# Optimization experiments

Hardware: AMD Instinct MI355X
Metric: run time of the kernel (lower is better)

## Reference

```python
import jax, jax.numpy as jnp
import numpy as np

N_HEADS, N_LEVELS, N_POINTS = 8, 4, 4


def _bilinear(im, grid, H, W):
    # im: [N, D, H*W] flattened level feature, grid: [N, Q, P, 2] in [-1, 1]
    # F.grid_sample bilinear, padding_mode='zeros', align_corners=False
    N, Q, P, _ = grid.shape
    D = im.shape[1]
    gx = ((grid[..., 0] + 1.0) * W - 1.0) * 0.5
    gy = ((grid[..., 1] + 1.0) * H - 1.0) * 0.5
    x0f = jnp.floor(gx)
    y0f = jnp.floor(gy)
    x0 = x0f.astype(jnp.int32)
    y0 = y0f.astype(jnp.int32)
    wx1 = gx - x0f
    wy1 = gy - y0f
    acc = jnp.zeros((N, D, Q * P), im.dtype)
    corners = ((0, 0, (1 - wx1) * (1 - wy1)), (1, 0, wx1 * (1 - wy1)),
               (0, 1, (1 - wx1) * wy1), (1, 1, wx1 * wy1))
    for dx, dy, wgt in corners:
        xi = x0 + dx
        yi = y0 + dy
        valid = (xi >= 0) & (xi < W) & (yi >= 0) & (yi < H)
        idx = jnp.clip(yi, 0, H - 1) * W + jnp.clip(xi, 0, W - 1)
        v = jnp.take_along_axis(im, idx.reshape(N, 1, Q * P), axis=2)  # [N,D,QP]
        acc = acc + v * jnp.where(valid, wgt, 0.0).reshape(N, 1, Q * P)
    return acc.reshape(N, D, Q, P)


def _forward(query, value, reference_points, shapes_np,
             w_off, b_off, w_attn, b_attn, w_val, b_val, w_out, b_out):
    B, Q, E = query.shape
    H_, L, P = N_HEADS, N_LEVELS, N_POINTS
    D = E // H_
    v = (value @ w_val + b_val).reshape(B, -1, H_, D)  # [B, Nv, H, D]
    off = (query @ w_off + b_off).reshape(B, Q, H_, L, P, 2)
    attn = (query @ w_attn + b_attn).reshape(B, Q, H_, L * P)
    attn = jax.nn.softmax(attn, axis=-1).reshape(B, Q, H_, L, P)
    # offset_scale = [W_l, H_l] per level
    scale = jnp.asarray(np.stack([shapes_np[:, 1], shapes_np[:, 0]], -1), jnp.float32)
    locs = reference_points[:, :, None, :, None, :] + off / scale[None, None, None, :, None, :]
    grid = 2.0 * locs - 1.0  # [B, Q, H, L, P, 2]
    starts = np.concatenate([[0], np.cumsum(shapes_np[:, 0] * shapes_np[:, 1])]).astype(int)
    out = jnp.zeros((B * H_, D, Q), query.dtype)
    for lvl in range(L):
        h, w = int(shapes_np[lvl, 0]), int(shapes_np[lvl, 1])
        feat = v[:, starts[lvl]:starts[lvl + 1]]                      # [B, h*w, H, D]
        feat = feat.transpose(0, 2, 3, 1).reshape(B * H_, D, h * w)   # [BH, D, hw]
        g = jnp.transpose(grid[:, :, :, lvl], (0, 2, 1, 3, 4)).reshape(B * H_, Q, P, 2)
        sampled = _bilinear(feat, g, h, w)                            # [BH, D, Q, P]
        wl = jnp.transpose(attn[:, :, :, lvl], (0, 2, 1, 3)).reshape(B * H_, 1, Q, P)
        out = out + (sampled * wl).sum(-1)                            # [BH, D, Q]
    out = out.reshape(B, H_ * D, Q).transpose(0, 2, 1)                # [B, Q, E]
    return out @ w_out + b_out


def setup_inputs() -> dict:
    key = jax.random.key(0)
    ks = jax.random.split(key, 12)
    B, Q, E = 2, 19947, 256
    L, H_, P = N_LEVELS, N_HEADS, N_POINTS
    shapes = jnp.array([[100, 150], [50, 75], [25, 38], [13, 19]], dtype=jnp.int64)
    s = 0.02
    return {
        'query': jax.random.normal(ks[0], (B, Q, E), jnp.float32),
        'value': jax.random.normal(ks[1], (B, Q, E), jnp.float32),
        'reference_points': jax.random.uniform(ks[2], (B, Q, L, 2), jnp.float32),
        'spatial_shapes': shapes,
        'w_off': jax.random.normal(ks[3], (E, H_ * L * P * 2), jnp.float32) * s,
        'b_off': jax.random.normal(ks[4], (H_ * L * P * 2,), jnp.float32) * s,
        'w_attn': jax.random.normal(ks[5], (E, H_ * L * P), jnp.float32) * s,
        'b_attn': jax.random.normal(ks[6], (H_ * L * P,), jnp.float32) * s,
        'w_val': jax.random.normal(ks[7], (E, E), jnp.float32) * s,
        'b_val': jax.random.normal(ks[8], (E,), jnp.float32) * s,
        'w_out': jax.random.normal(ks[9], (E, E), jnp.float32) * s,
        'b_out': jax.random.normal(ks[10], (E,), jnp.float32) * s,
    }


def reference(query, value, reference_points, spatial_shapes,
              w_off, b_off, w_attn, b_attn, w_val, b_val, w_out, b_out):
    shapes_np = np.asarray(spatial_shapes)
    return _forward(query, value, reference_points, shapes_np,
                    w_off, b_off, w_attn, b_attn, w_val, b_val, w_out, b_out)
```

## Files before the change

kernel.cpp:

```cpp
#include <hip/hip_runtime.h>
#include <math.h>

#define B_    2
#define Q_    19947
#define E_    256
#define H_    8
#define D_    32
#define L_    4
#define P_    4

typedef _Float16 f16_t;
typedef f16_t f16x8 __attribute__((ext_vector_type(8)));
typedef f16_t f16x4 __attribute__((ext_vector_type(4)));
typedef float f32x4 __attribute__((ext_vector_type(4)));

__global__ __launch_bounds__(256)
void transpose_all(const float* __restrict__ w_val, const float* __restrict__ w_off,
                   const float* __restrict__ w_attn, const float* __restrict__ w_out,
                   f16_t* __restrict__ WtV, f16_t* __restrict__ WtQ,
                   f16_t* __restrict__ WtO)
{
    const float* in; f16_t* out; int N;
    switch (blockIdx.z) {
        case 0:  in = w_val;  out = WtV;             N = 256; break;
        case 1:  in = w_off;  out = WtQ;             N = 256; break;
        case 2:  in = w_attn; out = WtQ + 256 * 256; N = 128; break;
        default: in = w_out;  out = WtO;             N = 256; break;
    }
    const int nt = blockIdx.x * 32;
    if (nt >= N) return;
    const int kt = blockIdx.y * 32;

    __shared__ float tile[32][33];
    const int x  = threadIdx.x & 31;
    const int y0 = threadIdx.x >> 5;
    #pragma unroll
    for (int p = 0; p < 4; ++p)
        tile[y0 + p * 8][x] = in[(size_t)(kt + y0 + p * 8) * N + nt + x];
    __syncthreads();
    #pragma unroll
    for (int p = 0; p < 4; ++p)
        out[(size_t)(nt + y0 + p * 8) * 256 + kt + x] = (f16_t)tile[x][y0 + p * 8];
}

__global__ __launch_bounds__(256, 5)
void gemm_proj(const float* __restrict__ Aval, const float* __restrict__ Aqry,
               const f16_t* __restrict__ WtV, const f16_t* __restrict__ WtQ,
               const float* __restrict__ b_val, const float* __restrict__ b_off,
               const float* __restrict__ b_attn,
               f16_t* __restrict__ v_proj, float* __restrict__ off_b,
               float* __restrict__ attn_b, int M)
{
    constexpr int K = 256, BK = 32, NIT = K / BK;
    __shared__ __align__(16) f16_t As[2][64][40];
    __shared__ __align__(16) f16_t Bs[2][128][40];

    const int t    = threadIdx.x;
    const int m0   = blockIdx.x * 64;
    const int by   = blockIdx.y;
    const bool isVal = (by < 2);
    const float*  Af = isVal ? Aval : Aqry;
    const f16_t*  Wt = isVal ? WtV : WtQ;
    const int n0     = isVal ? by * 128 : (by - 2) * 128;

    const int lane = t & 63;
    const int w    = t >> 6;
    const int wm   = w & 1, wn = w >> 1;
    const int quad = lane >> 4, l16 = lane & 15;

    const int srow = t >> 2;
    const int skc  = (t & 3) * 8;

    f32x4 acc[2][4];
    #pragma unroll
    for (int i = 0; i < 2; ++i)
        #pragma unroll
        for (int j = 0; j < 4; ++j) {
            f32x4 z = {0.f, 0.f, 0.f, 0.f};
            acc[i][j] = z;
        }

    f16x8 aval;
    uint4 bval0, bval1;

    auto load_stage = [&](int k0) {
        const int gm = m0 + srow;
        if (gm < M) {
            const float4 v0 = *(const float4*)(Af + (size_t)gm * 256 + k0 + skc);
            const float4 v1 = *(const float4*)(Af + (size_t)gm * 256 + k0 + skc + 4);
            aval[0] = (f16_t)v0.x; aval[1] = (f16_t)v0.y;
            aval[2] = (f16_t)v0.z; aval[3] = (f16_t)v0.w;
            aval[4] = (f16_t)v1.x; aval[5] = (f16_t)v1.y;
            aval[6] = (f16_t)v1.z; aval[7] = (f16_t)v1.w;
        } else {
            #pragma unroll
            for (int i = 0; i < 8; ++i) aval[i] = (f16_t)0.f;
        }
        bval0 = *(const uint4*)(Wt + (size_t)(n0 + srow)      * 256 + k0 + skc);
        bval1 = *(const uint4*)(Wt + (size_t)(n0 + srow + 64) * 256 + k0 + skc);
    };
    auto store_stage = [&](int buf) {
        *(f16x8*)&As[buf][srow][skc]      = aval;
        *(uint4*)&Bs[buf][srow][skc]      = bval0;
        *(uint4*)&Bs[buf][srow + 64][skc] = bval1;
    };

    load_stage(0);
    store_stage(0);
    int cur = 0;

    #pragma unroll
    for (int it = 0; it < NIT; ++it) {
        __syncthreads();
        if (it + 1 < NIT)
            load_stage((it + 1) * BK);

        f16x8 af[2], bfr[4];
        #pragma unroll
        for (int i = 0; i < 2; ++i)
            af[i] = *(const f16x8*)&As[cur][wm * 32 + i * 16 + l16][quad * 8];
        #pragma unroll
        for (int j = 0; j < 4; ++j)
            bfr[j] = *(const f16x8*)&Bs[cur][wn * 64 + j * 16 + l16][quad * 8];
        #pragma unroll
        for (int i = 0; i < 2; ++i)
            #pragma unroll
            for (int j = 0; j < 4; ++j)
                acc[i][j] = __builtin_amdgcn_mfma_f32_16x16x32_f16(af[i], bfr[j], acc[i][j], 0, 0, 0);

        if (it + 1 < NIT)
            store_stage(cur ^ 1);
        cur ^= 1;
    }

    #pragma unroll
    for (int j = 0; j < 4; ++j) {
        const int gn = n0 + wn * 64 + j * 16 + l16;
        const float bv = isVal ? b_val[gn] : (gn < 256 ? b_off[gn] : b_attn[gn - 256]);
        #pragma unroll
        for (int i = 0; i < 2; ++i) {
            #pragma unroll
            for (int r = 0; r < 4; ++r) {
                const int gm = m0 + wm * 32 + i * 16 + quad * 4 + r;
                if (gm < M) {
                    const float val = acc[i][j][r] + bv;
                    if (isVal)
                        v_proj[(size_t)gm * 256 + gn] = (f16_t)val;
                    else if (gn < 256)
                        off_b[(size_t)gm * 256 + gn] = val;
                    else
                        attn_b[(size_t)gm * 128 + (gn - 256)] = val;
                }
            }
        }
    }
}

__global__ __launch_bounds__(256, 4)
void msda_fused(const f16_t* __restrict__ v,
                const float* __restrict__ off,
                const float* __restrict__ attn,
                const float* __restrict__ ref,
                const f16_t* __restrict__ WoT,
                const float* __restrict__ b_out,
                float* __restrict__ out,
                int BQ)
{
    constexpr int SH[4] = {100, 50, 25, 13};
    constexpr int SW[4] = {150, 75, 38, 19};
    constexpr int ST[4] = {0, 15000, 18750, 19700};

    __shared__ __align__(16) f16_t Samp[16][264];

    const int t   = threadIdx.x;
    const int bq0 = blockIdx.x * 16;

    #pragma unroll
    for (int r = 0; r < 2; ++r) {
        const int g    = t >> 2;
        const int qi   = (g >> 3) + r * 8;
        const int h    = g & 7;
        const int lane = t & 3;
        const int bq   = bq0 + qi;

        float acc[8] = {0.f, 0.f, 0.f, 0.f, 0.f, 0.f, 0.f, 0.f};

        if (bq < BQ) {
            const int b = bq / Q_;
            const f16_t* vbase = v + ((size_t)b * Q_) * E_ + h * D_ + lane * 8;
            const float* offp  = off  + (size_t)bq * 256 + h * 32;
            const float* attnp = attn + (size_t)bq * 128 + h * 16;

            float aw[16];
            #pragma unroll
            for (int i = 0; i < 4; ++i) {
                const float4 x = *(const float4*)(attnp + i * 4);
                aw[i*4+0] = x.x; aw[i*4+1] = x.y; aw[i*4+2] = x.z; aw[i*4+3] = x.w;
            }
            float mx = aw[0];
            #pragma unroll
            for (int i = 1; i < 16; ++i) mx = fmaxf(mx, aw[i]);
            float sum = 0.f;
            #pragma unroll
            for (int i = 0; i < 16; ++i) { aw[i] = expf(aw[i] - mx); sum += aw[i]; }
            const float inv = 1.f / sum;
            #pragma unroll
            for (int i = 0; i < 16; ++i) aw[i] *= inv;

            const float4 r01 = *(const float4*)(ref + (size_t)bq * 8);
            const float4 r23 = *(const float4*)(ref + (size_t)bq * 8 + 4);
            const float rx[4] = {r01.x, r01.z, r23.x, r23.z};
            const float ry[4] = {r01.y, r01.w, r23.y, r23.w};

            #pragma unroll
            for (int l = 0; l < L_; ++l) {
                const float fW = (float)SW[l], fH = (float)SH[l];
                const int   Ww = SW[l], Hh = SH[l], st = ST[l];
                #pragma unroll
                for (int pp = 0; pp < 2; ++pp) {
                    const float4 o2 = *(const float4*)(offp + l * 8 + pp * 4);
                    #pragma unroll
                    for (int q = 0; q < 2; ++q) {
                        const int   p  = pp * 2 + q;
                        const float ox = q ? o2.z : o2.x;
                        const float oy = q ? o2.w : o2.y;
                        const float wA = aw[l * 4 + p];
                        const float gx = fmaf(rx[l], fW, ox) - 0.5f;
                        const float gy = fmaf(ry[l], fH, oy) - 0.5f;
                        const float x0f = floorf(gx), y0f = floorf(gy);
                        const int   x0  = (int)x0f,   y0  = (int)y0f;
                        const float wx1 = gx - x0f,   wy1 = gy - y0f;
                        const float wx0 = 1.f - wx1,  wy0 = 1.f - wy1;

                        const float mxw0 = ((unsigned)x0     < (unsigned)Ww) ? wx0 : 0.f;
                        const float mxw1 = ((unsigned)(x0+1) < (unsigned)Ww) ? wx1 : 0.f;
                        const float myw0 = ((unsigned)y0     < (unsigned)Hh) ? wy0 : 0.f;
                        const float myw1 = ((unsigned)(y0+1) < (unsigned)Hh) ? wy1 : 0.f;
                        const int xc0 = min(max(x0, 0),     Ww - 1);
                        const int xc1 = min(max(x0 + 1, 0), Ww - 1);
                        const int yc0 = min(max(y0, 0),     Hh - 1);
                        const int yc1 = min(max(y0 + 1, 0), Hh - 1);

                        const float w00 = wA * mxw0 * myw0;
                        const float w10 = wA * mxw1 * myw0;
                        const float w01 = wA * mxw0 * myw1;
                        const float w11 = wA * mxw1 * myw1;

                        const f16x8 s00 = *(const f16x8*)(vbase + (size_t)(st + yc0 * Ww + xc0) * E_);
                        const f16x8 s10 = *(const f16x8*)(vbase + (size_t)(st + yc0 * Ww + xc1) * E_);
                        const f16x8 s01 = *(const f16x8*)(vbase + (size_t)(st + yc1 * Ww + xc0) * E_);
                        const f16x8 s11 = *(const f16x8*)(vbase + (size_t)(st + yc1 * Ww + xc1) * E_);

                        #pragma unroll
                        for (int c = 0; c < 8; ++c) {
                            acc[c] = fmaf(w00, (float)s00[c], acc[c]);
                            acc[c] = fmaf(w10, (float)s10[c], acc[c]);
                            acc[c] = fmaf(w01, (float)s01[c], acc[c]);
                            acc[c] = fmaf(w11, (float)s11[c], acc[c]);
                        }
                    }
                }
            }
        }

        f16x8 o;
        #pragma unroll
        for (int c = 0; c < 8; ++c) o[c] = (f16_t)acc[c];
        *(f16x8*)&Samp[qi][h * 32 + lane * 8] = o;
    }

    __syncthreads();

    const int lane = t & 63;
    const int w    = t >> 6;
    const int quad = lane >> 4, l16 = lane & 15;

    f16x8 af[8];
    #pragma unroll
    for (int kf = 0; kf < 8; ++kf)
        af[kf] = *(const f16x8*)&Samp[l16][kf * 32 + quad * 8];

    f32x4 acc4[4];
    #pragma unroll
    for (int j = 0; j < 4; ++j) {
        f32x4 z = {0.f, 0.f, 0.f, 0.f};
        acc4[j] = z;
    }

    #pragma unroll
    for (int j = 0; j < 4; ++j) {
        const int n = w * 64 + j * 16 + l16;
        const f16_t* bp = WoT + (size_t)n * 256 + quad * 8;
        #pragma unroll
        for (int kf = 0; kf < 8; ++kf) {
            const f16x8 bfr = *(const f16x8*)(bp + kf * 32);
            acc4[j] = __builtin_amdgcn_mfma_f32_16x16x32_f16(af[kf], bfr, acc4[j], 0, 0, 0);
        }
    }

    #pragma unroll
    for (int j = 0; j < 4; ++j) {
        const int n  = w * 64 + j * 16 + l16;
        const float bv = b_out[n];
        #pragma unroll
        for (int r = 0; r < 4; ++r) {
            const int gm = bq0 + quad * 4 + r;
            if (gm < BQ)
                out[(size_t)gm * 256 + n] = acc4[j][r] + bv;
        }
    }
}

extern "C" void kernel_launch(void* const* d_in, const int* in_sizes, int n_in,
                              void* d_out, int out_size, void* d_ws, size_t ws_size,
                              hipStream_t stream)
{
    const float* query  = (const float*)d_in[0];
    const float* value  = (const float*)d_in[1];
    const float* refpts = (const float*)d_in[2];
    const float* w_off  = (const float*)d_in[4];
    const float* b_off  = (const float*)d_in[5];
    const float* w_attn = (const float*)d_in[6];
    const float* b_attn = (const float*)d_in[7];
    const float* w_val  = (const float*)d_in[8];
    const float* b_val  = (const float*)d_in[9];
    const float* w_out  = (const float*)d_in[10];
    const float* b_out  = (const float*)d_in[11];
    float* out = (float*)d_out;

    const int BQ = B_ * Q_;

    char* ws = (char*)d_ws;
    f16_t* v_proj = (f16_t*)ws;                       ws += (size_t)BQ * 256 * 2;
    float* off_b  = (float*)ws;                       ws += (size_t)BQ * 256 * 4;
    float* attn_b = (float*)ws;                       ws += (size_t)BQ * 128 * 4;
    f16_t* WtV    = (f16_t*)ws;                       ws += (size_t)256 * 256 * 2;
    f16_t* WtQ    = (f16_t*)ws;                       ws += (size_t)384 * 256 * 2;
    f16_t* WtO    = (f16_t*)ws;

    const dim3 blk(256);

    transpose_all<<<dim3(8, 8, 4), blk, 0, stream>>>(w_val, w_off, w_attn, w_out,
                                                     WtV, WtQ, WtO);

    const int mg = (BQ + 63) / 64;

    gemm_proj<<<dim3(mg, 5), blk, 0, stream>>>(
        value, query, WtV, WtQ, b_val, b_off, b_attn,
        v_proj, off_b, attn_b, BQ);

    msda_fused<<<dim3((BQ + 15) / 16), blk, 0, stream>>>(
        v_proj, off_b, attn_b, refpts, WtO, b_out, out, BQ);
}
```

Measured before the change: 294.9 us.

## Split fused sampling+output GEMM into separate kernels and retile projection GEMM

The fused deformable-attention kernel is split into a sampling kernel, one thread group per query-head with higher occupancy, and a separate output-projection GEMM that stages WtO through LDS. The sampled values go through a new fp16 workspace buffer instead of shared memory. The projection GEMM is retiled to 32-row M tiles with wide N tiles (256 for value, 192 for query) and a 3-column grid, so fewer blocks re-read the A operand. Sampling also uses 32-bit vector indexing. The split costs an extra global round trip of the sampled tensor and one more kernel launch.

```diff
diff --git a/kernel.cpp b/kernel.cpp
--- a/kernel.cpp
+++ b/kernel.cpp
@@ -43,7 +43,7 @@
         out[(size_t)(nt + y0 + p * 8) * 256 + kt + x] = (f16_t)tile[x][y0 + p * 8];
 }
 
-__global__ __launch_bounds__(256, 5)
+__global__ __launch_bounds__(256, 4)
 void gemm_proj(const float* __restrict__ Aval, const float* __restrict__ Aqry,
                const f16_t* __restrict__ WtV, const f16_t* __restrict__ WtQ,
                const float* __restrict__ b_val, const float* __restrict__ b_off,
@@ -51,25 +51,29 @@
                f16_t* __restrict__ v_proj, float* __restrict__ off_b,
                float* __restrict__ attn_b, int M)
 {
-    constexpr int K = 256, BK = 32, NIT = K / BK;
-    __shared__ __align__(16) f16_t As[2][64][40];
-    __shared__ __align__(16) f16_t Bs[2][128][40];
-
-    const int t    = threadIdx.x;
-    const int m0   = blockIdx.x * 64;
-    const int by   = blockIdx.y;
-    const bool isVal = (by < 2);
-    const float*  Af = isVal ? Aval : Aqry;
-    const f16_t*  Wt = isVal ? WtV : WtQ;
-    const int n0     = isVal ? by * 128 : (by - 2) * 128;
+    constexpr int BK = 32, NIT = 8;
+    __shared__ __align__(16) f16_t As[2][32][40];
+    __shared__ __align__(16) f16_t Bs[2][256][40];
+
+    const int t  = threadIdx.x;
+    const int m0 = blockIdx.x * 32;
+    const int by = blockIdx.y;
+    const bool isVal = (by == 0);
+    const float* __restrict__ Af = isVal ? Aval : Aqry;
+    const f16_t* __restrict__ Wt = isVal ? WtV : WtQ;
+    const int n0  = isVal ? 0 : (by - 1) * 192;
+    const int NW  = isVal ? 256 : 192;
+    const int NWq = NW >> 2;
+    const int JW  = NWq >> 4;
 
     const int lane = t & 63;
-    const int w    = t >> 6;
-    const int wm   = w & 1, wn = w >> 1;
+    const int wn   = t >> 6;
     const int quad = lane >> 4, l16 = lane & 15;
 
-    const int srow = t >> 2;
-    const int skc  = (t & 3) * 8;
+    const int srow  = t >> 2;
+    const int skc   = (t & 3) * 8;
+    const int srowA = t >> 3;
+    const int skcA  = (t & 7) * 4;
 
     f32x4 acc[2][4];
     #pragma unroll
@@ -80,29 +84,30 @@
             acc[i][j] = z;
         }
 
-    f16x8 aval;
-    uint4 bval0, bval1;
+    f16x4 aval;
+    uint4 bval[4];
 
     auto load_stage = [&](int k0) {
-        const int gm = m0 + srow;
+        const int gm = m0 + srowA;
         if (gm < M) {
-            const float4 v0 = *(const float4*)(Af + (size_t)gm * 256 + k0 + skc);
-            const float4 v1 = *(const float4*)(Af + (size_t)gm * 256 + k0 + skc + 4);
+            const float4 v0 = *(const float4*)(Af + (size_t)gm * 256 + k0 + skcA);
             aval[0] = (f16_t)v0.x; aval[1] = (f16_t)v0.y;
             aval[2] = (f16_t)v0.z; aval[3] = (f16_t)v0.w;
-            aval[4] = (f16_t)v1.x; aval[5] = (f16_t)v1.y;
-            aval[6] = (f16_t)v1.z; aval[7] = (f16_t)v1.w;
         } else {
             #pragma unroll
-            for (int i = 0; i < 8; ++i) aval[i] = (f16_t)0.f;
-        }
-        bval0 = *(const uint4*)(Wt + (size_t)(n0 + srow)      * 256 + k0 + skc);
-        bval1 = *(const uint4*)(Wt + (size_t)(n0 + srow + 64) * 256 + k0 + skc);
+            for (int i = 0; i < 4; ++i) aval[i] = (f16_t)0.f;
+        }
+        #pragma unroll
+        for (int s = 0; s < 4; ++s)
+            if (s * 64 < NW)
+                bval[s] = *(const uint4*)(Wt + (size_t)(n0 + s * 64 + srow) * 256 + k0 + skc);
     };
     auto store_stage = [&](int buf) {
-        *(f16x8*)&As[buf][srow][skc]      = aval;
-        *(uint4*)&Bs[buf][srow][skc]      = bval0;
-        *(uint4*)&Bs[buf][srow + 64][skc] = bval1;
+        *(f16x4*)&As[buf][srowA][skcA] = aval;
+        #pragma unroll
+        for (int s = 0; s < 4; ++s)
+            if (s * 64 < NW)
+                *(uint4*)&Bs[buf][s * 64 + srow][skc] = bval[s];
     };
 
     load_stage(0);
@@ -115,18 +120,19 @@
         if (it + 1 < NIT)
             load_stage((it + 1) * BK);
 
-        f16x8 af[2], bfr[4];
+        f16x8 af[2];
         #pragma unroll
         for (int i = 0; i < 2; ++i)
-            af[i] = *(const f16x8*)&As[cur][wm * 32 + i * 16 + l16][quad * 8];
-        #pragma unroll
-        for (int j = 0; j < 4; ++j)
-            bfr[j] = *(const f16x8*)&Bs[cur][wn * 64 + j * 16 + l16][quad * 8];
-        #pragma unroll
-        for (int i = 0; i < 2; ++i)
-            #pragma unroll
-            for (int j = 0; j < 4; ++j)
-                acc[i][j] = __builtin_amdgcn_mfma_f32_16x16x32_f16(af[i], bfr[j], acc[i][j], 0, 0, 0);
+            af[i] = *(const f16x8*)&As[cur][i * 16 + l16][quad * 8];
+        #pragma unroll
+        for (int j = 0; j < 4; ++j) {
+            if (j < JW) {
+                const f16x8 bfr = *(const f16x8*)&Bs[cur][wn * NWq + j * 16 + l16][quad * 8];
+                #pragma unroll
+                for (int i = 0; i < 2; ++i)
+                    acc[i][j] = __builtin_amdgcn_mfma_f32_16x16x32_f16(af[i], bfr, acc[i][j], 0, 0, 0);
+            }
+        }
 
         if (it + 1 < NIT)
             store_stage(cur ^ 1);
@@ -135,178 +141,227 @@
 
     #pragma unroll
     for (int j = 0; j < 4; ++j) {
-        const int gn = n0 + wn * 64 + j * 16 + l16;
-        const float bv = isVal ? b_val[gn] : (gn < 256 ? b_off[gn] : b_attn[gn - 256]);
-        #pragma unroll
-        for (int i = 0; i < 2; ++i) {
-            #pragma unroll
-            for (int r = 0; r < 4; ++r) {
-                const int gm = m0 + wm * 32 + i * 16 + quad * 4 + r;
-                if (gm < M) {
-                    const float val = acc[i][j][r] + bv;
-                    if (isVal)
-                        v_proj[(size_t)gm * 256 + gn] = (f16_t)val;
-                    else if (gn < 256)
-                        off_b[(size_t)gm * 256 + gn] = val;
-                    else
-                        attn_b[(size_t)gm * 128 + (gn - 256)] = val;
+        if (j < JW) {
+            const int nl = wn * NWq + j * 16 + l16;
+            const int gq = n0 + nl;
+            const float bv = isVal ? b_val[nl] : (gq < 256 ? b_off[gq] : b_attn[gq - 256]);
+            #pragma unroll
+            for (int i = 0; i < 2; ++i) {
+                #pragma unroll
+                for (int r = 0; r < 4; ++r) {
+                    const int gm = m0 + i * 16 + quad * 4 + r;
+                    if (gm < M) {
+                        const float val = acc[i][j][r] + bv;
+                        if (isVal)
+                            v_proj[(size_t)gm * 256 + nl] = (f16_t)val;
+                        else if (gq < 256)
+                            off_b[(size_t)gm * 256 + gq] = val;
+                        else
+                            attn_b[(size_t)gm * 128 + (gq - 256)] = val;
+                    }
                 }
             }
         }
     }
 }
 
-__global__ __launch_bounds__(256, 4)
-void msda_fused(const f16_t* __restrict__ v,
-                const float* __restrict__ off,
-                const float* __restrict__ attn,
-                const float* __restrict__ ref,
-                const f16_t* __restrict__ WoT,
-                const float* __restrict__ b_out,
-                float* __restrict__ out,
-                int BQ)
+__global__ __launch_bounds__(256, 8)
+void msda_sample(const f16_t* __restrict__ v,
+                 const float* __restrict__ off,
+                 const float* __restrict__ attn,
+                 const float* __restrict__ ref,
+                 f16_t* __restrict__ samp,
+                 int BQ)
 {
     constexpr int SH[4] = {100, 50, 25, 13};
     constexpr int SW[4] = {150, 75, 38, 19};
     constexpr int ST[4] = {0, 15000, 18750, 19700};
 
-    __shared__ __align__(16) f16_t Samp[16][264];
-
-    const int t   = threadIdx.x;
-    const int bq0 = blockIdx.x * 16;
-
-    #pragma unroll
-    for (int r = 0; r < 2; ++r) {
-        const int g    = t >> 2;
-        const int qi   = (g >> 3) + r * 8;
-        const int h    = g & 7;
-        const int lane = t & 3;
-        const int bq   = bq0 + qi;
-
-        float acc[8] = {0.f, 0.f, 0.f, 0.f, 0.f, 0.f, 0.f, 0.f};
-
-        if (bq < BQ) {
-            const int b = bq / Q_;
-            const f16_t* vbase = v + ((size_t)b * Q_) * E_ + h * D_ + lane * 8;
-            const float* offp  = off  + (size_t)bq * 256 + h * 32;
-            const float* attnp = attn + (size_t)bq * 128 + h * 16;
-
-            float aw[16];
-            #pragma unroll
-            for (int i = 0; i < 4; ++i) {
-                const float4 x = *(const float4*)(attnp + i * 4);
-                aw[i*4+0] = x.x; aw[i*4+1] = x.y; aw[i*4+2] = x.z; aw[i*4+3] = x.w;
-            }
-            float mx = aw[0];
-            #pragma unroll
-            for (int i = 1; i < 16; ++i) mx = fmaxf(mx, aw[i]);
-            float sum = 0.f;
-            #pragma unroll
-            for (int i = 0; i < 16; ++i) { aw[i] = expf(aw[i] - mx); sum += aw[i]; }
-            const float inv = 1.f / sum;
-            #pragma unroll
-            for (int i = 0; i < 16; ++i) aw[i] *= inv;
-
-            const float4 r01 = *(const float4*)(ref + (size_t)bq * 8);
-            const float4 r23 = *(const float4*)(ref + (size_t)bq * 8 + 4);
-            const float rx[4] = {r01.x, r01.z, r23.x, r23.z};
-            const float ry[4] = {r01.y, r01.w, r23.y, r23.w};
-
-            #pragma unroll
-            for (int l = 0; l < L_; ++l) {
-                const float fW = (float)SW[l], fH = (float)SH[l];
-                const int   Ww = SW[l], Hh = SH[l], st = ST[l];
+    const int t    = threadIdx.x;
+    const int g    = blockIdx.x * 64 + (t >> 2);
+    const int lane = t & 3;
+    const int bq   = g >> 3;
+    const int h    = g & 7;
+    if (bq >= BQ) return;
+
+    const f16x8* __restrict__ vp = (const f16x8*)v;
+    const unsigned int hoff = (unsigned int)(h * 4 + lane)
+                            + (bq >= Q_ ? (unsigned int)(Q_ * E_ / 8) : 0u);
+
+    const float* __restrict__ offp  = off  + (size_t)bq * 256 + h * 32;
+    const float* __restrict__ attnp = attn + (size_t)bq * 128 + h * 16;
+
+    float aw[16];
+    #pragma unroll
+    for (int i = 0; i < 4; ++i) {
+        const float4 x = *(const float4*)(attnp + i * 4);
+        aw[i*4+0] = x.x; aw[i*4+1] = x.y; aw[i*4+2] = x.z; aw[i*4+3] = x.w;
+    }
+    float mx = aw[0];
+    #pragma unroll
+    for (int i = 1; i < 16; ++i) mx = fmaxf(mx, aw[i]);
+    float sum = 0.f;
+    #pragma unroll
+    for (int i = 0; i < 16; ++i) { aw[i] = expf(aw[i] - mx); sum += aw[i]; }
+    const float inv = 1.f / sum;
+    #pragma unroll
+    for (int i = 0; i < 16; ++i) aw[i] *= inv;
+
+    const float4 r01 = *(const float4*)(ref + (size_t)bq * 8);
+    const float4 r23 = *(const float4*)(ref + (size_t)bq * 8 + 4);
+    const float rx[4] = {r01.x, r01.z, r23.x, r23.z};
+    const float ry[4] = {r01.y, r01.w, r23.y, r23.w};
+
+    float acc[8] = {0.f, 0.f, 0.f, 0.f, 0.f, 0.f, 0.f, 0.f};
+
+    #pragma unroll
+    for (int l = 0; l < L_; ++l) {
+        const float fW = (float)SW[l], fH = (float)SH[l];
+        const int   Ww = SW[l], Hh = SH[l], st = ST[l];
+        #pragma unroll
+        for (int pp = 0; pp < 2; ++pp) {
+            const float4 o2 = *(const float4*)(offp + l * 8 + pp * 4);
+            #pragma unroll
+            for (int q = 0; q < 2; ++q) {
+                const int   p  = pp * 2 + q;
+                const float ox = q ? o2.z : o2.x;
+                const float oy = q ? o2.w : o2.y;
+                const float wA = aw[l * 4 + p];
+                const float gx = fmaf(rx[l], fW, ox) - 0.5f;
+                const float gy = fmaf(ry[l], fH, oy) - 0.5f;
+                const float x0f = floorf(gx), y0f = floorf(gy);
+                const int   x0  = (int)x0f,   y0  = (int)y0f;
+                const float wx1 = gx - x0f,   wy1 = gy - y0f;
+                const float wx0 = 1.f - wx1,  wy0 = 1.f - wy1;
+
+                const float mxw0 = ((unsigned)x0     < (unsigned)Ww) ? wx0 : 0.f;
+                const float mxw1 = ((unsigned)(x0+1) < (unsigned)Ww) ? wx1 : 0.f;
+                const float myw0 = ((unsigned)y0     < (unsigned)Hh) ? wy0 : 0.f;
+                const float myw1 = ((unsigned)(y0+1) < (unsigned)Hh) ? wy1 : 0.f;
+                const int xc0 = min(max(x0, 0),     Ww - 1);
+                const int xc1 = min(max(x0 + 1, 0), Ww - 1);
+                const int yc0 = min(max(y0, 0),     Hh - 1);
+                const int yc1 = min(max(y0 + 1, 0), Hh - 1);
+
+                const float w00 = wA * mxw0 * myw0;
+                const float w10 = wA * mxw1 * myw0;
+                const float w01 = wA * mxw0 * myw1;
+                const float w11 = wA * mxw1 * myw1;
+
+                const unsigned int row0 = (unsigned int)(st + yc0 * Ww) * 32u + hoff;
+                const unsigned int row1 = (unsigned int)(st + yc1 * Ww) * 32u + hoff;
+                const f16x8 s00 = vp[row0 + (unsigned int)xc0 * 32u];
+                const f16x8 s10 = vp[row0 + (unsigned int)xc1 * 32u];
+                const f16x8 s01 = vp[row1 + (unsigned int)xc0 * 32u];
+                const f16x8 s11 = vp[row1 + (unsigned int)xc1 * 32u];
+
                 #pragma unroll
-                for (int pp = 0; pp < 2; ++pp) {
-                    const float4 o2 = *(const float4*)(offp + l * 8 + pp * 4);
-                    #pragma unroll
-                    for (int q = 0; q < 2; ++q) {
-                        const int   p  = pp * 2 + q;
-                        const float ox = q ? o2.z : o2.x;
-                        const float oy = q ? o2.w : o2.y;
-                        const float wA = aw[l * 4 + p];
-                        const float gx = fmaf(rx[l], fW, ox) - 0.5f;
-                        const float gy = fmaf(ry[l], fH, oy) - 0.5f;
-                        const float x0f = floorf(gx), y0f = floorf(gy);
-                        const int   x0  = (int)x0f,   y0  = (int)y0f;
-                        const float wx1 = gx - x0f,   wy1 = gy - y0f;
-                        const float wx0 = 1.f - wx1,  wy0 = 1.f - wy1;
-
-                        const float mxw0 = ((unsigned)x0     < (unsigned)Ww) ? wx0 : 0.f;
-                        const float mxw1 = ((unsigned)(x0+1) < (unsigned)Ww) ? wx1 : 0.f;
-                        const float myw0 = ((unsigned)y0     < (unsigned)Hh) ? wy0 : 0.f;
-                        const float myw1 = ((unsigned)(y0+1) < (unsigned)Hh) ? wy1 : 0.f;
-                        const int xc0 = min(max(x0, 0),     Ww - 1);
-                        const int xc1 = min(max(x0 + 1, 0), Ww - 1);
-                        const int yc0 = min(max(y0, 0),     Hh - 1);
-                        const int yc1 = min(max(y0 + 1, 0), Hh - 1);
-
-                        const float w00 = wA * mxw0 * myw0;
-                        const float w10 = wA * mxw1 * myw0;
-                        const float w01 = wA * mxw0 * myw1;
-                        const float w11 = wA * mxw1 * myw1;
-
-                        const f16x8 s00 = *(const f16x8*)(vbase + (size_t)(st + yc0 * Ww + xc0) * E_);
-                        const f16x8 s10 = *(const f16x8*)(vbase + (size_t)(st + yc0 * Ww + xc1) * E_);
-                        const f16x8 s01 = *(const f16x8*)(vbase + (size_t)(st + yc1 * Ww + xc0) * E_);
-                        const f16x8 s11 = *(const f16x8*)(vbase + (size_t)(st + yc1 * Ww + xc1) * E_);
-
-                        #pragma unroll
-                        for (int c = 0; c < 8; ++c) {
-                            acc[c] = fmaf(w00, (float)s00[c], acc[c]);
-                            acc[c] = fmaf(w10, (float)s10[c], acc[c]);
-                            acc[c] = fmaf(w01, (float)s01[c], acc[c]);
-                            acc[c] = fmaf(w11, (float)s11[c], acc[c]);
-                        }
-                    }
+                for (int c = 0; c < 8; ++c) {
+                    acc[c] = fmaf(w00, (float)s00[c], acc[c]);
+                    acc[c] = fmaf(w10, (float)s10[c], acc[c]);
+                    acc[c] = fmaf(w01, (float)s01[c], acc[c]);
+                    acc[c] = fmaf(w11, (float)s11[c], acc[c]);
                 }
             }
         }
-
-        f16x8 o;
-        #pragma unroll
-        for (int c = 0; c < 8; ++c) o[c] = (f16_t)acc[c];
-        *(f16x8*)&Samp[qi][h * 32 + lane * 8] = o;
-    }
-
-    __syncthreads();
+    }
+
+    f16x8 o;
+    #pragma unroll
+    for (int c = 0; c < 8; ++c) o[c] = (f16_t)acc[c];
+    *(f16x8*)(samp + (size_t)bq * 256 + h * 32 + lane * 8) = o;
+}
+
+__global__ __launch_bounds__(256, 4)
+void gemm_out(const f16_t* __restrict__ A, const f16_t* __restrict__ WtO,
+              const float* __restrict__ b_out, float* __restrict__ out, int M)
+{
+    constexpr int BK = 32, NIT = 8;
+    __shared__ __align__(16) f16_t As[2][32][40];
+    __shared__ __align__(16) f16_t Bs[2][256][40];
+
+    const int t  = threadIdx.x;
+    const int m0 = blockIdx.x * 32;
 
     const int lane = t & 63;
-    const int w    = t >> 6;
+    const int wn   = t >> 6;
     const int quad = lane >> 4, l16 = lane & 15;
 
-    f16x8 af[8];
-    #pragma unroll
-    for (int kf = 0; kf < 8; ++kf)
-        af[kf] = *(const f16x8*)&Samp[l16][kf * 32 + quad * 8];
-
-    f32x4 acc4[4];
+    const int srow  = t >> 2;
+    const int skc   = (t & 3) * 8;
+    const int srowA = t >> 3;
+    const int skcA  = (t & 7) * 4;
+
+    f32x4 acc[2][4];
+    #pragma unroll
+    for (int i = 0; i < 2; ++i)
+        #pragma unroll
+        for (int j = 0; j < 4; ++j) {
+            f32x4 z = {0.f, 0.f, 0.f, 0.f};
+            acc[i][j] = z;
+        }
+
+    f16x4 aval;
+    uint4 bval[4];
+
+    auto load_stage = [&](int k0) {
+        const int gm = m0 + srowA;
+        if (gm < M) {
+            aval = *(const f16x4*)(A + (size_t)gm * 256 + k0 + skcA);
+        } else {
+            #pragma unroll
+            for (int i = 0; i < 4; ++i) aval[i] = (f16_t)0.f;
+        }
+        #pragma unroll
+        for (int s = 0; s < 4; ++s)
+            bval[s] = *(const uint4*)(WtO + (size_t)(s * 64 + srow) * 256 + k0 + skc);
+    };
+    auto store_stage = [&](int buf) {
+        *(f16x4*)&As[buf][srowA][skcA] = aval;
+        #pragma unroll
+        for (int s = 0; s < 4; ++s)
+            *(uint4*)&Bs[buf][s * 64 + srow][skc] = bval[s];
+    };
+
+    load_stage(0);
+    store_stage(0);
+    int cur = 0;
+
+    #pragma unroll
+    for (int it = 0; it < NIT; ++it) {
+        __syncthreads();
+        if (it + 1 < NIT)
+            load_stage((it + 1) * BK);
+
+        f16x8 af[2];
+        #pragma unroll
+        for (int i = 0; i < 2; ++i)
+            af[i] = *(const f16x8*)&As[cur][i * 16 + l16][quad * 8];
+        #pragma unroll
+        for (int j = 0; j < 4; ++j) {
+            const f16x8 bfr = *(const f16x8*)&Bs[cur][wn * 64 + j * 16 + l16][quad * 8];
+            #pragma unroll
+            for (int i = 0; i < 2; ++i)
+                acc[i][j] = __builtin_amdgcn_mfma_f32_16x16x32_f16(af[i], bfr, acc[i][j], 0, 0, 0);
+        }
+
+        if (it + 1 < NIT)
+            store_stage(cur ^ 1);
+        cur ^= 1;
+    }
+
     #pragma unroll
     for (int j = 0; j < 4; ++j) {
-        f32x4 z = {0.f, 0.f, 0.f, 0.f};
-        acc4[j] = z;
-    }
-
-    #pragma unroll
-    for (int j = 0; j < 4; ++j) {
-        const int n = w * 64 + j * 16 + l16;
-        const f16_t* bp = WoT + (size_t)n * 256 + quad * 8;
-        #pragma unroll
-        for (int kf = 0; kf < 8; ++kf) {
-            const f16x8 bfr = *(const f16x8*)(bp + kf * 32);
-            acc4[j] = __builtin_amdgcn_mfma_f32_16x16x32_f16(af[kf], bfr, acc4[j], 0, 0, 0);
-        }
-    }
-
-    #pragma unroll
-    for (int j = 0; j < 4; ++j) {
-        const int n  = w * 64 + j * 16 + l16;
-        const float bv = b_out[n];
-        #pragma unroll
-        for (int r = 0; r < 4; ++r) {
-            const int gm = bq0 + quad * 4 + r;
-            if (gm < BQ)
-                out[(size_t)gm * 256 + n] = acc4[j][r] + bv;
+        const int gn = wn * 64 + j * 16 + l16;
+        const float bv = b_out[gn];
+        #pragma unroll
+        for (int i = 0; i < 2; ++i) {
+            #pragma unroll
+            for (int r = 0; r < 4; ++r) {
+                const int gm = m0 + i * 16 + quad * 4 + r;
+                if (gm < M)
+                    out[(size_t)gm * 256 + gn] = acc[i][j][r] + bv;
+            }
         }
     }
 }
@@ -334,6 +389,7 @@
     f16_t* v_proj = (f16_t*)ws;                       ws += (size_t)BQ * 256 * 2;
     float* off_b  = (float*)ws;                       ws += (size_t)BQ * 256 * 4;
     float* attn_b = (float*)ws;                       ws += (size_t)BQ * 128 * 4;
+    f16_t* samp   = (f16_t*)ws;                       ws += (size_t)BQ * 256 * 2;
     f16_t* WtV    = (f16_t*)ws;                       ws += (size_t)256 * 256 * 2;
     f16_t* WtQ    = (f16_t*)ws;                       ws += (size_t)384 * 256 * 2;
     f16_t* WtO    = (f16_t*)ws;
@@ -343,12 +399,15 @@
     transpose_all<<<dim3(8, 8, 4), blk, 0, stream>>>(w_val, w_off, w_attn, w_out,
                                                      WtV, WtQ, WtO);
 
-    const int mg = (BQ + 63) / 64;
-
-    gemm_proj<<<dim3(mg, 5), blk, 0, stream>>>(
+    const int mg32 = (BQ + 31) / 32;
+
+    gemm_proj<<<dim3(mg32, 3), blk, 0, stream>>>(
         value, query, WtV, WtQ, b_val, b_off, b_attn,
         v_proj, off_b, attn_b, BQ);
 
-    msda_fused<<<dim3((BQ + 15) / 16), blk, 0, stream>>>(
-        v_proj, off_b, attn_b, refpts, WtO, b_out, out, BQ);
+    const int sg = (BQ * 32 + 255) / 256;
+    msda_sample<<<dim3(sg), blk, 0, stream>>>(
+        v_proj, off_b, attn_b, refpts, samp, BQ);
+
+    gemm_out<<<dim3(mg32), blk, 0, stream>>>(samp, WtO, b_out, out, BQ);
 }
```

After: 451.2 us. 53.0% more time.

## Replace tiled projection GEMM with 16-row tiles streaming weights from global

Applied to the files above, without the earlier changes.

The double-buffered 64x128 LDS-tiled projection GEMM is replaced by a kernel where each block loads a 16-row slab of activations (full K=256) into LDS once. Each warp then streams its slice of the transposed fp16 weights directly from global/L2 into MFMA operands. Each block covers all output columns of one projection, so the A rows are read once instead of once per column tile. The cost is that weights are re-read from cache by every block and B-operand reuse through LDS is lost.

```diff
diff --git a/kernel.cpp b/kernel.cpp
--- a/kernel.cpp
+++ b/kernel.cpp
@@ -43,113 +43,90 @@
         out[(size_t)(nt + y0 + p * 8) * 256 + kt + x] = (f16_t)tile[x][y0 + p * 8];
 }
 
-__global__ __launch_bounds__(256, 5)
-void gemm_proj(const float* __restrict__ Aval, const float* __restrict__ Aqry,
-               const f16_t* __restrict__ WtV, const f16_t* __restrict__ WtQ,
-               const float* __restrict__ b_val, const float* __restrict__ b_off,
-               const float* __restrict__ b_attn,
-               f16_t* __restrict__ v_proj, float* __restrict__ off_b,
-               float* __restrict__ attn_b, int M)
+__global__ __launch_bounds__(256, 4)
+void gemm_rowtile(const float* __restrict__ Aval, const float* __restrict__ Aqry,
+                  const f16_t* __restrict__ WtV, const f16_t* __restrict__ WtQ,
+                  const float* __restrict__ b_val, const float* __restrict__ b_off,
+                  const float* __restrict__ b_attn,
+                  f16_t* __restrict__ v_proj, float* __restrict__ off_b,
+                  float* __restrict__ attn_b, int M)
 {
-    constexpr int K = 256, BK = 32, NIT = K / BK;
-    __shared__ __align__(16) f16_t As[2][64][40];
-    __shared__ __align__(16) f16_t Bs[2][128][40];
-
-    const int t    = threadIdx.x;
-    const int m0   = blockIdx.x * 64;
-    const int by   = blockIdx.y;
-    const bool isVal = (by < 2);
-    const float*  Af = isVal ? Aval : Aqry;
-    const f16_t*  Wt = isVal ? WtV : WtQ;
-    const int n0     = isVal ? by * 128 : (by - 2) * 128;
+    __shared__ __align__(16) f16_t As[16][264];
+
+    const int t  = threadIdx.x;
+    const int m0 = blockIdx.x * 16;
+    const bool isVal = (blockIdx.y == 0);
+    const float* __restrict__ Af = isVal ? Aval : Aqry;
+    const f16_t* __restrict__ Wt = isVal ? WtV : WtQ;
+    const int NWq = isVal ? 64 : 96;
+    const int JW  = isVal ? 4 : 6;
+
+    {
+        const int r  = t >> 4;
+        const int c0 = (t & 15) * 16;
+        const int gm = m0 + r;
+        f16_t tmp[16];
+        if (gm < M) {
+            #pragma unroll
+            for (int u = 0; u < 4; ++u) {
+                const float4 v4 = *(const float4*)(Af + (size_t)gm * 256 + c0 + u * 4);
+                tmp[u*4+0] = (f16_t)v4.x; tmp[u*4+1] = (f16_t)v4.y;
+                tmp[u*4+2] = (f16_t)v4.z; tmp[u*4+3] = (f16_t)v4.w;
+            }
+        } else {
+            #pragma unroll
+            for (int u = 0; u < 16; ++u) tmp[u] = (f16_t)0.f;
+        }
+        *(f16x8*)&As[r][c0]     = *(const f16x8*)&tmp[0];
+        *(f16x8*)&As[r][c0 + 8] = *(const f16x8*)&tmp[8];
+    }
+    __syncthreads();
 
     const int lane = t & 63;
     const int w    = t >> 6;
-    const int wm   = w & 1, wn = w >> 1;
     const int quad = lane >> 4, l16 = lane & 15;
 
-    const int srow = t >> 2;
-    const int skc  = (t & 3) * 8;
-
-    f32x4 acc[2][4];
-    #pragma unroll
-    for (int i = 0; i < 2; ++i)
-        #pragma unroll
-        for (int j = 0; j < 4; ++j) {
-            f32x4 z = {0.f, 0.f, 0.f, 0.f};
-            acc[i][j] = z;
-        }
-
-    f16x8 aval;
-    uint4 bval0, bval1;
-
-    auto load_stage = [&](int k0) {
-        const int gm = m0 + srow;
-        if (gm < M) {
-            const float4 v0 = *(const float4*)(Af + (size_t)gm * 256 + k0 + skc);
-            const float4 v1 = *(const float4*)(Af + (size_t)gm * 256 + k0 + skc + 4);
-            aval[0] = (f16_t)v0.x; aval[1] = (f16_t)v0.y;
-            aval[2] = (f16_t)v0.z; aval[3] = (f16_t)v0.w;
-            aval[4] = (f16_t)v1.x; aval[5] = (f16_t)v1.y;
-            aval[6] = (f16_t)v1.z; aval[7] = (f16_t)v1.w;
-        } else {
-            #pragma unroll
-            for (int i = 0; i < 8; ++i) aval[i] = (f16_t)0.f;
-        }
-        bval0 = *(const uint4*)(Wt + (size_t)(n0 + srow)      * 256 + k0 + skc);
-        bval1 = *(const uint4*)(Wt + (size_t)(n0 + srow + 64) * 256 + k0 + skc);
-    };
-    auto store_stage = [&](int buf) {
-        *(f16x8*)&As[buf][srow][skc]      = aval;
-        *(uint4*)&Bs[buf][srow][skc]      = bval0;
-        *(uint4*)&Bs[buf][srow + 64][skc] = bval1;
-    };
-
-    load_stage(0);
-    store_stage(0);
-    int cur = 0;
-
-    #pragma unroll
-    for (int it = 0; it < NIT; ++it) {
-        __syncthreads();
-        if (it + 1 < NIT)
-            load_stage((it + 1) * BK);
-
-        f16x8 af[2], bfr[4];
-        #pragma unroll
-        for (int i = 0; i < 2; ++i)
-            af[i] = *(const f16x8*)&As[cur][wm * 32 + i * 16 + l16][quad * 8];
-        #pragma unroll
-        for (int j = 0; j < 4; ++j)
-            bfr[j] = *(const f16x8*)&Bs[cur][wn * 64 + j * 16 + l16][quad * 8];
-        #pragma unroll
-        for (int i = 0; i < 2; ++i)
-            #pragma unroll
-            for (int j = 0; j < 4; ++j)
-                acc[i][j] = __builtin_amdgcn_mfma_f32_16x16x32_f16(af[i], bfr[j], acc[i][j], 0, 0, 0);
-
-        if (it + 1 < NIT)
-            store_stage(cur ^ 1);
-        cur ^= 1;
-    }
-
-    #pragma unroll
-    for (int j = 0; j < 4; ++j) {
-        const int gn = n0 + wn * 64 + j * 16 + l16;
-        const float bv = isVal ? b_val[gn] : (gn < 256 ? b_off[gn] : b_attn[gn - 256]);
-        #pragma unroll
-        for (int i = 0; i < 2; ++i) {
+    f16x8 af[8];
+    #pragma unroll
+    for (int kf = 0; kf < 8; ++kf)
+        af[kf] = *(const f16x8*)&As[l16][kf * 32 + quad * 8];
+
+    f32x4 acc[6];
+    #pragma unroll
+    for (int j = 0; j < 6; ++j) {
+        f32x4 z = {0.f, 0.f, 0.f, 0.f};
+        acc[j] = z;
+    }
+
+    #pragma unroll
+    for (int j = 0; j < 6; ++j) {
+        if (j < JW) {
+            const int n = w * NWq + j * 16 + l16;
+            const f16_t* bp = Wt + (size_t)n * 256 + quad * 8;
+            #pragma unroll
+            for (int kf = 0; kf < 8; ++kf) {
+                const f16x8 bfr = *(const f16x8*)(bp + kf * 32);
+                acc[j] = __builtin_amdgcn_mfma_f32_16x16x32_f16(af[kf], bfr, acc[j], 0, 0, 0);
+            }
+        }
+    }
+
+    #pragma unroll
+    for (int j = 0; j < 6; ++j) {
+        if (j < JW) {
+            const int n = w * NWq + j * 16 + l16;
+            const float bv = isVal ? b_val[n] : (n < 256 ? b_off[n] : b_attn[n - 256]);
             #pragma unroll
             for (int r = 0; r < 4; ++r) {
-                const int gm = m0 + wm * 32 + i * 16 + quad * 4 + r;
+                const int gm = m0 + quad * 4 + r;
                 if (gm < M) {
-                    const float val = acc[i][j][r] + bv;
+                    const float val = acc[j][r] + bv;
                     if (isVal)
-                        v_proj[(size_t)gm * 256 + gn] = (f16_t)val;
-                    else if (gn < 256)
-                        off_b[(size_t)gm * 256 + gn] = val;
+                        v_proj[(size_t)gm * 256 + n] = (f16_t)val;
+                    else if (n < 256)
+                        off_b[(size_t)gm * 256 + n] = val;
                     else
-                        attn_b[(size_t)gm * 128 + (gn - 256)] = val;
+                        attn_b[(size_t)gm * 128 + (n - 256)] = val;
                 }
             }
         }
@@ -343,12 +320,12 @@
     transpose_all<<<dim3(8, 8, 4), blk, 0, stream>>>(w_val, w_off, w_attn, w_out,
                                                      WtV, WtQ, WtO);
 
-    const int mg = (BQ + 63) / 64;
-
-    gemm_proj<<<dim3(mg, 5), blk, 0, stream>>>(
+    const int mg16 = (BQ + 15) / 16;
+
+    gemm_rowtile<<<dim3(mg16, 2), blk, 0, stream>>>(
         value, query, WtV, WtQ, b_val, b_off, b_attn,
         v_proj, off_b, attn_b, BQ);
 
-    msda_fused<<<dim3((BQ + 15) / 16), blk, 0, stream>>>(
+    msda_fused<<<dim3(mg16), blk, 0, stream>>>(
         v_proj, off_b, attn_b, refpts, WtO, b_out, out, BQ);
 }
```

Measured after the change: 348.9 us. 18.3% more time.
